# Performance work log

Measured on AMD Instinct MI355X. Metric: run time of the kernel, lower is better.

The kernel has to match this reference:

```python
import jax, jax.numpy as jnp
import numpy as np
import math

B, S, D = 2, 4096, 512
H = 8
DH = D // H  # 64


def setup_inputs() -> dict:
    key = jax.random.key(0)
    k1, k2, k3, k4, k5 = jax.random.split(key, 5)
    scale = 1.0 / math.sqrt(D)
    return {
        "x": jax.random.normal(k1, (B, S, D), dtype=jnp.float32),
        "W_in": jax.random.normal(k2, (D, 3 * D), dtype=jnp.float32) * scale,
        "b_in": jax.random.normal(k3, (3 * D,), dtype=jnp.float32) * 0.01,
        "W_out": jax.random.normal(k4, (D, D), dtype=jnp.float32) * scale,
        "b_out": jax.random.normal(k5, (D,), dtype=jnp.float32) * 0.01,
        "causal_mask": 1,
    }


def reference(x, W_in, b_in, W_out, b_out, causal_mask):
    b, s, d = x.shape
    # fused QKV projection: (b, s, 3d)
    qkv = x @ W_in + b_in
    q, k, v = jnp.split(qkv, 3, axis=-1)
    # (b, s, d) -> (b, h, s, dh)
    def to_heads(t):
        return t.reshape(b, s, H, DH).transpose(0, 2, 1, 3)
    q, k, v = to_heads(q), to_heads(k), to_heads(v)
    # raw scores (b, h, s, s)
    scores = jnp.einsum("bhqd,bhkd->bhqk", q, k)
    if causal_mask:  # static python flag
        # upper-triangular (strictly above diag) -> -inf, applied pre-scaling
        # (matches source; -inf invariant under /sqrt(d_head))
        tri = jnp.triu(jnp.ones((s, s), dtype=bool), k=1)
        scores = jnp.where(tri, -jnp.inf, scores)
    attn = jax.nn.softmax(scores / math.sqrt(DH), axis=-1)
    out = jnp.einsum("bhqk,bhkd->bhqd", attn, v)
    out = out.transpose(0, 2, 1, 3).reshape(b, s, d)
    return out @ W_out + b_out
```

## Files before the change

### kernel.cpp

```cpp
#include <hip/hip_runtime.h>
#include <cstdint>
#include <cmath>

typedef unsigned short BF16;
typedef __attribute__((ext_vector_type(8))) short short8;
typedef __attribute__((ext_vector_type(4))) float f32x4;
typedef __attribute__((ext_vector_type(16))) float f32x16;
typedef __attribute__((ext_vector_type(2))) unsigned int uint2v;
typedef __attribute__((ext_vector_type(4))) unsigned int uint4v;

#define S_LEN 4096
#define DMODEL 512
#define NHEAD 8
#define DHEAD 64
#define BS 2
#define NROWS (BS * NHEAD * S_LEN)

__device__ __forceinline__ BF16 f2bf(float f) {
  union { float f; uint32_t u; } v; v.f = f;
  uint32_t r = (v.u + 0x7FFFu + ((v.u >> 16) & 1u)) >> 16;
  return (BF16)r;
}

__device__ __forceinline__ float bf2f(short u) {
  return __uint_as_float(((unsigned)(unsigned short)u) << 16);
}

__device__ __forceinline__ unsigned cvtpk(float a, float b) {
  unsigned r;
  asm volatile("v_cvt_pk_bf16_f32 %0, %1, %2" : "=v"(r) : "v"(a), "v"(b));
  return r;
}

__device__ __forceinline__ float partner32(float x, int hi) {
  unsigned a = __float_as_uint(x), b = a;
  uint2v r = __builtin_amdgcn_permlane32_swap(a, b, false, false);
  return __uint_as_float(hi ? r[0] : r[1]);
}

__device__ __forceinline__ void pl32(unsigned &a, unsigned &b) {
  uint2v r = __builtin_amdgcn_permlane32_swap(a, b, false, false);
  a = r[0]; b = r[1];
}

__device__ __forceinline__ void gload16(const void* g, void* lds) {
  __builtin_amdgcn_global_load_lds(
      (const __attribute__((address_space(1))) void*)g,
      (__attribute__((address_space(3))) void*)lds, 16, 0, 0);
}

#define MAX3(a, b, c) fmaxf(fmaxf((a), (b)), (c))
#define CS_CONST 0.18033688011112042f

__global__ __launch_bounds__(256) void cvt_x_k(const float* __restrict__ x,
                                               BF16* __restrict__ xb) {
  int i = blockIdx.x * 256 + threadIdx.x;
  float4 v = reinterpret_cast<const float4*>(x)[i];
  ushort4 o;
  o.x = f2bf(v.x); o.y = f2bf(v.y); o.z = f2bf(v.z); o.w = f2bf(v.w);
  reinterpret_cast<ushort4*>(xb)[i] = o;
}

__global__ __launch_bounds__(256) void trw_k(const float* __restrict__ W_in,
                                             const float* __restrict__ W_out,
                                             BF16* __restrict__ wint,
                                             BF16* __restrict__ woutt) {
  __shared__ float t[32][33];
  const bool second = blockIdx.x >= 48;
  const float* W = second ? W_out : W_in;
  BF16* Wt = second ? woutt : wint;
  const int N = second ? DMODEL : 3 * DMODEL;
  const int K = DMODEL;
  int n0 = (second ? ((int)blockIdx.x - 48) : (int)blockIdx.x) * 32;
  int k0 = blockIdx.y * 32;
  int tx = threadIdx.x & 31, ty = threadIdx.x >> 5;
#pragma unroll
  for (int i = 0; i < 4; ++i)
    t[ty + 8 * i][tx] = W[(size_t)(k0 + ty + 8 * i) * N + n0 + tx];
  __syncthreads();
#pragma unroll
  for (int i = 0; i < 4; ++i)
    Wt[(size_t)(n0 + ty + 8 * i) * K + k0 + tx] = f2bf(t[tx][ty + 8 * i]);
}

template <int MODE>
__global__ __launch_bounds__(256)
void gemm_k(const BF16* __restrict__ A, const BF16* __restrict__ Bt,
            const float* __restrict__ bias,
            BF16* __restrict__ Qb, BF16* __restrict__ Kb, BF16* __restrict__ Vc,
            float* __restrict__ Out) {
  __shared__ BF16 As[128 * 64];
  __shared__ BF16 Bs[128 * 64];
  const int tid = threadIdx.x;
  const int l = tid & 63, w = tid >> 6;
  const int wm = w >> 1, wn = w & 1;
  const int bm = blockIdx.x, bn = blockIdx.y;
  f32x4 acc[4][4] = {};

  for (int kt = 0; kt < 512 / 64; ++kt) {
#pragma unroll
    for (int i = 0; i < 4; ++i) {
      int ldsoff = i * 4096 + w * 1024;
      int off = ldsoff + l * 16;
      int row = off >> 7;
      int slot = ((off >> 4) & 7) ^ (row & 7);
      gload16(A + (size_t)(bm * 128 + row) * 512 + kt * 64 + slot * 8,
              (char*)As + ldsoff);
      gload16(Bt + (size_t)(bn * 128 + row) * 512 + kt * 64 + slot * 8,
              (char*)Bs + ldsoff);
    }
    __syncthreads();
    const char* Ab = (const char*)As;
    const char* Bb = (const char*)Bs;
    short8 af[4][2], bfr[4][2];
#pragma unroll
    for (int mf = 0; mf < 4; ++mf)
#pragma unroll
      for (int kk = 0; kk < 2; ++kk) {
        int row = wm * 64 + mf * 16 + (l & 15);
        int slot = ((l >> 4) + 4 * kk) ^ (row & 7);
        af[mf][kk] = *(const short8*)(Ab + row * 128 + slot * 16);
      }
#pragma unroll
    for (int nf = 0; nf < 4; ++nf)
#pragma unroll
      for (int kk = 0; kk < 2; ++kk) {
        int row = wn * 64 + nf * 16 + (l & 15);
        int slot = ((l >> 4) + 4 * kk) ^ (row & 7);
        bfr[nf][kk] = *(const short8*)(Bb + row * 128 + slot * 16);
      }
    __builtin_amdgcn_s_setprio(1);
#pragma unroll
    for (int kk = 0; kk < 2; ++kk)
#pragma unroll
      for (int mf = 0; mf < 4; ++mf)
#pragma unroll
        for (int nf = 0; nf < 4; ++nf)
          acc[mf][nf] = __builtin_amdgcn_mfma_f32_16x16x32_bf16(
              af[mf][kk], bfr[nf][kk], acc[mf][nf], 0, 0, 0);
    __builtin_amdgcn_s_setprio(0);
    __syncthreads();
  }

#pragma unroll
  for (int mf = 0; mf < 4; ++mf)
#pragma unroll
    for (int nf = 0; nf < 4; ++nf)
#pragma unroll
      for (int r = 0; r < 4; ++r) {
        int row = bm * 128 + wm * 64 + mf * 16 + ((l >> 4) << 2) + r;
        int col = bn * 128 + wn * 64 + nf * 16 + (l & 15);
        float v = acc[mf][nf][r] + bias[col];
        if (MODE == 0) {
          int sec = col >> 9, nl = col & 511;
          int h = nl >> 6, dh = nl & 63;
          int b = row >> 12, s = row & 4095;
          BF16* dst = sec == 0 ? Qb : (sec == 1 ? Kb : Vc);
          dst[(((size_t)(b * NHEAD + h)) * S_LEN + s) * DHEAD + dh] = f2bf(v);
        } else {
          Out[(size_t)row * DMODEL + col] = v;
        }
      }
}

__global__ __launch_bounds__(256)
void v_tr_k(const BF16* __restrict__ Vc, BF16* __restrict__ Vt) {
  __shared__ BF16 t[64][66];
  const int bh = blockIdx.y, st = blockIdx.x;
  const int tid = threadIdx.x;
  const int g = tid >> 3, c8 = (tid & 7) * 8;
#pragma unroll
  for (int p = 0; p < 2; ++p) {
    int s = p * 32 + g;
    short8 v = *(const short8*)(Vc + ((size_t)bh * S_LEN + st * 64 + s) * DHEAD + c8);
#pragma unroll
    for (int j = 0; j < 8; ++j) t[s][c8 + j] = (BF16)(unsigned short)v[j];
  }
  __syncthreads();
#pragma unroll
  for (int p = 0; p < 2; ++p) {
    int dh = p * 32 + g;
    short8 o;
#pragma unroll
    for (int j = 0; j < 8; ++j) o[j] = (short)t[c8 + j][dh];
    *(short8*)(Vt + ((size_t)bh * DHEAD + dh) * S_LEN + st * 64 + c8) = o;
  }
}

__global__ __launch_bounds__(256, 4)
void attn_k(const BF16* __restrict__ Qg, const BF16* __restrict__ Kg,
            const BF16* __restrict__ Vg, BF16* __restrict__ Opb,
            float* __restrict__ Ml) {
  __shared__ BF16 Kl[2][64 * 64];
  __shared__ BF16 Vl[2][64 * 64];
  const int tid = threadIdx.x, l = tid & 63, w = tid >> 6;
  const int hi = l >> 5, ln = l & 31;
  const int wgid = blockIdx.x;
  const int xcd = wgid & 7, j = wgid >> 3;
  const int bh = xcd * 2 + (j & 1);
  const int qr = (j >> 1) & 3;
  const int p = j >> 3;
  const BF16* Qh = Qg + (size_t)bh * S_LEN * DHEAD;
  const BF16* Kh = Kg + (size_t)bh * S_LEN * DHEAD;
  const BF16* Vh = Vg + (size_t)bh * DHEAD * S_LEN;
  const float CS = CS_CONST;

  int cur = 0;
  for (int rep = 0; rep < 2; ++rep) {
    const int qt = rep ? (31 - p) : p;
    const int qq = rep ? (3 - qr) : qr;
    const int NTf = 2 * qt + 2;
    const int kbase = (qq * NTf) >> 2;
    const int kend = ((qq + 1) * NTf) >> 2;
    const int NT = kend - kbase;
    const int q0w = qt * 128 + w * 32;
    const int qrow = q0w + ln;
    __syncthreads();

    short8 qb[4];
    {
      const BF16* qp = Qh + (size_t)qrow * DHEAD + hi * 8;
#pragma unroll
      for (int ks = 0; ks < 4; ++ks) qb[ks] = *(const short8*)(qp + ks * 16);
    }
    f32x16 oacc0 = {}, oacc1 = {};
    float m_ = -INFINITY, l_ = 0.f;

    auto stage = [&](int buf, int ktile) {
      const int kv0 = ktile * 64;
#pragma unroll
      for (int i = 0; i < 2; ++i) {
        int base = i * 4096 + w * 1024;
        int off = base + l * 16;
        int row = off >> 7;
        int slot = ((off >> 4) & 7) ^ (row & 7);
        gload16(Kh + (size_t)(kv0 + row) * DHEAD + slot * 8, (char*)Kl[buf] + base);
        gload16(Vh + (size_t)row * S_LEN + kv0 + slot * 8, (char*)Vl[buf] + base);
      }
    };

    if (NT > 0) {
      stage(cur, kbase);
      for (int kt = 0; kt < NT; ++kt) {
        __syncthreads();
        if (kt + 1 < NT) stage(cur ^ 1, kbase + kt + 1);
        const int kv0 = (kbase + kt) * 64;
        if (kv0 <= q0w + 31) {
          const char* Kb_ = (const char*)Kl[cur];
          f32x16 s0 = {}, s1 = {};
          __builtin_amdgcn_s_setprio(1);
#pragma unroll
          for (int ks = 0; ks < 4; ++ks) {
            int slot0 = (2 * ks + hi) ^ (ln & 7);
            short8 kf0 = *(const short8*)(Kb_ + ln * 128 + slot0 * 16);
            int row1 = 32 + ln;
            int slot1 = (2 * ks + hi) ^ (row1 & 7);
            short8 kf1 = *(const short8*)(Kb_ + row1 * 128 + slot1 * 16);
            s0 = __builtin_amdgcn_mfma_f32_32x32x16_bf16(kf0, qb[ks], s0, 0, 0, 0);
            s1 = __builtin_amdgcn_mfma_f32_32x32x16_bf16(kf1, qb[ks], s1, 0, 0, 0);
          }
          __builtin_amdgcn_s_setprio(0);
          if (kv0 + 63 > q0w) {
#pragma unroll
            for (int r = 0; r < 16; ++r) {
              int crow = (r & 3) + 8 * (r >> 2) + 4 * hi;
              if (kv0 + crow > qrow) s0[r] = -INFINITY;
              if (kv0 + 32 + crow > qrow) s1[r] = -INFINITY;
            }
          }
          float a0 = MAX3(s0[0], s0[1], s0[2]);
          float a1 = MAX3(s0[3], s0[4], s0[5]);
          float a2 = MAX3(s0[6], s0[7], s0[8]);
          float a3 = MAX3(s0[9], s0[10], s0[11]);
          float a4 = MAX3(s0[12], s0[13], s0[14]);
          float a5 = MAX3(s0[15], s1[0], s1[1]);
          float a6 = MAX3(s1[2], s1[3], s1[4]);
          float a7 = MAX3(s1[5], s1[6], s1[7]);
          float a8 = MAX3(s1[8], s1[9], s1[10]);
          float a9 = MAX3(s1[11], s1[12], s1[13]);
          float a10 = fmaxf(s1[14], s1[15]);
          float b0 = MAX3(a0, a1, a2);
          float b1 = MAX3(a3, a4, a5);
          float b2 = MAX3(a6, a7, a8);
          float b3 = fmaxf(a9, a10);
          float pmax = fmaxf(fmaxf(b0, b1), fmaxf(b2, b3));
          pmax = fmaxf(pmax, partner32(pmax, hi));
          bool need = (pmax - m_) * CS > 8.0f;
          if (__any(need)) {
            float mn = fmaxf(m_, pmax);
            float alpha = exp2f((m_ - mn) * CS);
            m_ = mn;
            l_ *= alpha;
#pragma unroll
            for (int r = 0; r < 16; ++r) { oacc0[r] *= alpha; oacc1[r] *= alpha; }
          }
          const float mb = m_ * CS;
          float p0[16], p1[16];
          float rs = 0.f;
#pragma unroll
          for (int r = 0; r < 16; ++r) { p0[r] = exp2f(fmaf(s0[r], CS, -mb)); rs += p0[r]; }
#pragma unroll
          for (int r = 0; r < 16; ++r) { p1[r] = exp2f(fmaf(s1[r], CS, -mb)); rs += p1[r]; }
          rs += partner32(rs, hi);
          l_ += rs;
          short8 pf[4];
#pragma unroll
          for (int hf = 0; hf < 2; ++hf) {
            const float* pp = hf ? p1 : p0;
            unsigned w01 = cvtpk(pp[0], pp[1]), w23 = cvtpk(pp[2], pp[3]);
            unsigned w45 = cvtpk(pp[4], pp[5]), w67 = cvtpk(pp[6], pp[7]);
            unsigned w89 = cvtpk(pp[8], pp[9]), wab = cvtpk(pp[10], pp[11]);
            unsigned wcd = cvtpk(pp[12], pp[13]), wef = cvtpk(pp[14], pp[15]);
            pl32(w01, w45);
            pl32(w23, w67);
            pl32(w89, wcd);
            pl32(wab, wef);
            union { uint4v u; short8 s; } c0, c1;
            c0.u = (uint4v){w01, w23, w45, w67};
            c1.u = (uint4v){w89, wab, wcd, wef};
            pf[hf * 2 + 0] = c0.s;
            pf[hf * 2 + 1] = c1.s;
          }
          const char* Vb_ = (const char*)Vl[cur];
          __builtin_amdgcn_s_setprio(1);
#pragma unroll
          for (int ks = 0; ks < 4; ++ks) {
            int slot0 = (2 * ks + hi) ^ (ln & 7);
            short8 vf0 = *(const short8*)(Vb_ + ln * 128 + slot0 * 16);
            int row1 = 32 + ln;
            int slot1 = (2 * ks + hi) ^ (row1 & 7);
            short8 vf1 = *(const short8*)(Vb_ + row1 * 128 + slot1 * 16);
            oacc0 = __builtin_amdgcn_mfma_f32_32x32x16_bf16(vf0, pf[ks], oacc0, 0, 0, 0);
            oacc1 = __builtin_amdgcn_mfma_f32_32x32x16_bf16(vf1, pf[ks], oacc1, 0, 0, 0);
          }
          __builtin_amdgcn_s_setprio(0);
        }
        cur ^= 1;
      }
    }

    BF16* Op = Opb + ((size_t)qq * NROWS + (size_t)bh * S_LEN + qrow) * DHEAD;
#pragma unroll
    for (int blk = 0; blk < 2; ++blk) {
      const f32x16 oa = blk ? oacc1 : oacc0;
#pragma unroll
      for (int g = 0; g < 4; ++g) {
        int dh0 = 8 * g + 4 * hi + 32 * blk;
        unsigned lo = cvtpk(oa[4 * g + 0], oa[4 * g + 1]);
        unsigned h2 = cvtpk(oa[4 * g + 2], oa[4 * g + 3]);
        uint2v st = {lo, h2};
        *(uint2v*)(Op + dh0) = st;
      }
    }
    if (hi == 0) {
      float2 ml = {m_, l_};
      *(float2*)(Ml + ((size_t)qq * NROWS + (size_t)bh * S_LEN + qrow) * 2) = ml;
    }
  }
}

__global__ __launch_bounds__(256)
void merge_k(const BF16* __restrict__ Opb, const float* __restrict__ Ml,
             BF16* __restrict__ Ob) {
  const int wv = blockIdx.x * 4 + (threadIdx.x >> 6);
  const int lane = threadIdx.x & 63;
  const int r_off = lane >> 3, c8 = (lane & 7) * 8;
#pragma unroll
  for (int it = 0; it < 4; ++it) {
    int row = wv * 32 + it * 8 + r_off;
    float2 ml0 = *(const float2*)(Ml + (size_t)row * 2);
    float2 ml1 = *(const float2*)(Ml + ((size_t)NROWS + row) * 2);
    float2 ml2 = *(const float2*)(Ml + ((size_t)2 * NROWS + row) * 2);
    float2 ml3 = *(const float2*)(Ml + ((size_t)3 * NROWS + row) * 2);
    float m = fmaxf(fmaxf(ml0.x, ml1.x), fmaxf(ml2.x, ml3.x));
    float a0 = exp2f((ml0.x - m) * CS_CONST);
    float a1 = exp2f((ml1.x - m) * CS_CONST);
    float a2 = exp2f((ml2.x - m) * CS_CONST);
    float a3 = exp2f((ml3.x - m) * CS_CONST);
    float linv = 1.0f / (ml0.y * a0 + ml1.y * a1 + ml2.y * a2 + ml3.y * a3);
    a0 *= linv; a1 *= linv; a2 *= linv; a3 *= linv;
    short8 v0 = *(const short8*)(Opb + ((size_t)0 * NROWS + row) * DHEAD + c8);
    short8 v1 = *(const short8*)(Opb + ((size_t)1 * NROWS + row) * DHEAD + c8);
    short8 v2 = *(const short8*)(Opb + ((size_t)2 * NROWS + row) * DHEAD + c8);
    short8 v3 = *(const short8*)(Opb + ((size_t)3 * NROWS + row) * DHEAD + c8);
    float o[8];
#pragma unroll
    for (int jj = 0; jj < 8; ++jj)
      o[jj] = bf2f(v0[jj]) * a0 + bf2f(v1[jj]) * a1 +
              bf2f(v2[jj]) * a2 + bf2f(v3[jj]) * a3;
    uint4v pk = {cvtpk(o[0], o[1]), cvtpk(o[2], o[3]),
                 cvtpk(o[4], o[5]), cvtpk(o[6], o[7])};
    int bh = row >> 12, s = row & 4095;
    *(uint4v*)(Ob + ((size_t)((bh >> 3) * S_LEN + s)) * DMODEL +
               (bh & 7) * DHEAD + c8) = pk;
  }
}

extern "C" void kernel_launch(void* const* d_in, const int* in_sizes, int n_in,
                              void* d_out, int out_size, void* d_ws, size_t ws_size,
                              hipStream_t stream) {
  const float* x = (const float*)d_in[0];
  const float* W_in = (const float*)d_in[1];
  const float* b_in = (const float*)d_in[2];
  const float* W_out = (const float*)d_in[3];
  const float* b_out = (const float*)d_in[4];
  float* out = (float*)d_out;

  char* ws = (char*)d_ws;
  const size_t SZ_X = (size_t)BS * S_LEN * DMODEL * 2;
  const size_t SZ_OP = (size_t)NROWS * DHEAD * 2;
  BF16* xb    = (BF16*)(ws);
  BF16* Vt    = xb;
  BF16* wint  = (BF16*)(ws + SZ_X);
  BF16* woutt = (BF16*)(ws + SZ_X + 3 * DMODEL * DMODEL * 2);
  BF16* Qb    = (BF16*)(ws + SZ_X + 4 * DMODEL * DMODEL * 2);
  BF16* Kb    = (BF16*)((char*)Qb + SZ_X);
  BF16* Vc    = (BF16*)((char*)Kb + SZ_X);
  BF16* Ob    = (BF16*)((char*)Vc + SZ_X);
  BF16* Opb   = (BF16*)((char*)Ob + SZ_X);
  float* Ml   = (float*)((char*)Opb + 4 * SZ_OP);

  cvt_x_k<<<dim3((BS * S_LEN * DMODEL) / 4 / 256), 256, 0, stream>>>(x, xb);
  trw_k<<<dim3(64, DMODEL / 32), 256, 0, stream>>>(W_in, W_out, wint, woutt);
  gemm_k<0><<<dim3(BS * S_LEN / 128, 3 * DMODEL / 128), 256, 0, stream>>>(
      xb, wint, b_in, Qb, Kb, Vc, nullptr);
  v_tr_k<<<dim3(S_LEN / 64, BS * NHEAD), 256, 0, stream>>>(Vc, Vt);
  attn_k<<<dim3(1024), 256, 0, stream>>>(Qb, Kb, Vt, Opb, Ml);
  merge_k<<<dim3(512), 256, 0, stream>>>(Opb, Ml, Ob);
  gemm_k<1><<<dim3(BS * S_LEN / 128, DMODEL / 128), 256, 0, stream>>>(
      Ob, woutt, b_out, nullptr, nullptr, nullptr, out);
}
```

Baseline: 193.7 us.

## Fuse V transpose into QKV GEMM epilogue and merge prep kernels

The QKV GEMM now writes V directly in transposed (head, dh, seq) layout. It stages each V tile through the A/B shared-memory buffers and stores 16-byte vectors, which removes the separate v_tr_k kernel and its round trip through global memory. The x conversion and weight transpose kernels are merged into one launch, saving a kernel launch. The workspace layout is reshuffled so Ob aliases xb. The risk is extra LDS traffic and a barrier in the V-block epilogue.

```diff
diff --git a/kernel.cpp b/kernel.cpp
--- a/kernel.cpp
+++ b/kernel.cpp
@@ -52,27 +52,29 @@
 #define MAX3(a, b, c) fmaxf(fmaxf((a), (b)), (c))
 #define CS_CONST 0.18033688011112042f
 
-__global__ __launch_bounds__(256) void cvt_x_k(const float* __restrict__ x,
-                                               BF16* __restrict__ xb) {
-  int i = blockIdx.x * 256 + threadIdx.x;
-  float4 v = reinterpret_cast<const float4*>(x)[i];
-  ushort4 o;
-  o.x = f2bf(v.x); o.y = f2bf(v.y); o.z = f2bf(v.z); o.w = f2bf(v.w);
-  reinterpret_cast<ushort4*>(xb)[i] = o;
-}
-
-__global__ __launch_bounds__(256) void trw_k(const float* __restrict__ W_in,
-                                             const float* __restrict__ W_out,
-                                             BF16* __restrict__ wint,
-                                             BF16* __restrict__ woutt) {
+__global__ __launch_bounds__(256)
+void prep_k(const float* __restrict__ x, const float* __restrict__ W_in,
+            const float* __restrict__ W_out, BF16* __restrict__ xb,
+            BF16* __restrict__ wint, BF16* __restrict__ woutt) {
   __shared__ float t[32][33];
-  const bool second = blockIdx.x >= 48;
+  const int bx = blockIdx.x;
+  if (bx < 4096) {
+    int i = bx * 256 + threadIdx.x;
+    float4 v = reinterpret_cast<const float4*>(x)[i];
+    ushort4 o;
+    o.x = f2bf(v.x); o.y = f2bf(v.y); o.z = f2bf(v.z); o.w = f2bf(v.w);
+    reinterpret_cast<ushort4*>(xb)[i] = o;
+    return;
+  }
+  const int tb = bx - 4096;
+  const int bxx = tb & 63, byy = tb >> 6;
+  const bool second = bxx >= 48;
   const float* W = second ? W_out : W_in;
   BF16* Wt = second ? woutt : wint;
   const int N = second ? DMODEL : 3 * DMODEL;
   const int K = DMODEL;
-  int n0 = (second ? ((int)blockIdx.x - 48) : (int)blockIdx.x) * 32;
-  int k0 = blockIdx.y * 32;
+  int n0 = (second ? (bxx - 48) : bxx) * 32;
+  int k0 = byy * 32;
   int tx = threadIdx.x & 31, ty = threadIdx.x >> 5;
 #pragma unroll
   for (int i = 0; i < 4; ++i)
@@ -87,7 +89,7 @@
 __global__ __launch_bounds__(256)
 void gemm_k(const BF16* __restrict__ A, const BF16* __restrict__ Bt,
             const float* __restrict__ bias,
-            BF16* __restrict__ Qb, BF16* __restrict__ Kb, BF16* __restrict__ Vc,
+            BF16* __restrict__ Qb, BF16* __restrict__ Kb, BF16* __restrict__ Vt,
             float* __restrict__ Out) {
   __shared__ BF16 As[128 * 64];
   __shared__ BF16 Bs[128 * 64];
@@ -142,6 +144,39 @@
     __syncthreads();
   }
 
+  if (MODE == 0 && bn >= 8) {
+#pragma unroll
+    for (int mf = 0; mf < 4; ++mf)
+#pragma unroll
+      for (int nf = 0; nf < 4; ++nf)
+#pragma unroll
+        for (int r = 0; r < 4; ++r) {
+          int rloc = wm * 64 + mf * 16 + ((l >> 4) << 2) + r;
+          int col = bn * 128 + wn * 64 + nf * 16 + (l & 15);
+          float v = acc[mf][nf][r] + bias[col];
+          int nl = col & 511;
+          int hh = (nl >> 6) & 1;
+          int dh = nl & 63;
+          BF16* T = hh ? Bs : As;
+          T[dh * 128 + rloc] = f2bf(v);
+        }
+    __syncthreads();
+    const int dh_grp = tid >> 4;
+    const int soff = (tid & 15) * 8;
+    const int b = bm >> 5, s0 = (bm & 31) * 128;
+#pragma unroll
+    for (int it = 0; it < 8; ++it) {
+      int dhh = it * 16 + dh_grp;
+      int head = dhh >> 6, dh = dhh & 63;
+      const BF16* T = head ? Bs : As;
+      short8 vv = *(const short8*)(T + dh * 128 + soff);
+      int hglob = (bn - 8) * 2 + head;
+      *(short8*)(Vt + (((size_t)(b * NHEAD + hglob)) * DHEAD + dh) * S_LEN +
+                 s0 + soff) = vv;
+    }
+    return;
+  }
+
 #pragma unroll
   for (int mf = 0; mf < 4; ++mf)
 #pragma unroll
@@ -155,36 +190,12 @@
           int sec = col >> 9, nl = col & 511;
           int h = nl >> 6, dh = nl & 63;
           int b = row >> 12, s = row & 4095;
-          BF16* dst = sec == 0 ? Qb : (sec == 1 ? Kb : Vc);
+          BF16* dst = sec == 0 ? Qb : Kb;
           dst[(((size_t)(b * NHEAD + h)) * S_LEN + s) * DHEAD + dh] = f2bf(v);
         } else {
           Out[(size_t)row * DMODEL + col] = v;
         }
       }
-}
-
-__global__ __launch_bounds__(256)
-void v_tr_k(const BF16* __restrict__ Vc, BF16* __restrict__ Vt) {
-  __shared__ BF16 t[64][66];
-  const int bh = blockIdx.y, st = blockIdx.x;
-  const int tid = threadIdx.x;
-  const int g = tid >> 3, c8 = (tid & 7) * 8;
-#pragma unroll
-  for (int p = 0; p < 2; ++p) {
-    int s = p * 32 + g;
-    short8 v = *(const short8*)(Vc + ((size_t)bh * S_LEN + st * 64 + s) * DHEAD + c8);
-#pragma unroll
-    for (int j = 0; j < 8; ++j) t[s][c8 + j] = (BF16)(unsigned short)v[j];
-  }
-  __syncthreads();
-#pragma unroll
-  for (int p = 0; p < 2; ++p) {
-    int dh = p * 32 + g;
-    short8 o;
-#pragma unroll
-    for (int j = 0; j < 8; ++j) o[j] = (short)t[c8 + j][dh];
-    *(short8*)(Vt + ((size_t)bh * DHEAD + dh) * S_LEN + st * 64 + c8) = o;
-  }
 }
 
 __global__ __launch_bounds__(256, 4)
@@ -410,21 +421,18 @@
   const size_t SZ_X = (size_t)BS * S_LEN * DMODEL * 2;
   const size_t SZ_OP = (size_t)NROWS * DHEAD * 2;
   BF16* xb    = (BF16*)(ws);
-  BF16* Vt    = xb;
+  BF16* Ob    = xb;
   BF16* wint  = (BF16*)(ws + SZ_X);
   BF16* woutt = (BF16*)(ws + SZ_X + 3 * DMODEL * DMODEL * 2);
   BF16* Qb    = (BF16*)(ws + SZ_X + 4 * DMODEL * DMODEL * 2);
   BF16* Kb    = (BF16*)((char*)Qb + SZ_X);
-  BF16* Vc    = (BF16*)((char*)Kb + SZ_X);
-  BF16* Ob    = (BF16*)((char*)Vc + SZ_X);
-  BF16* Opb   = (BF16*)((char*)Ob + SZ_X);
+  BF16* Vt    = (BF16*)((char*)Kb + SZ_X);
+  BF16* Opb   = (BF16*)((char*)Vt + SZ_X);
   float* Ml   = (float*)((char*)Opb + 4 * SZ_OP);
 
-  cvt_x_k<<<dim3((BS * S_LEN * DMODEL) / 4 / 256), 256, 0, stream>>>(x, xb);
-  trw_k<<<dim3(64, DMODEL / 32), 256, 0, stream>>>(W_in, W_out, wint, woutt);
+  prep_k<<<dim3(4096 + 1024), 256, 0, stream>>>(x, W_in, W_out, xb, wint, woutt);
   gemm_k<0><<<dim3(BS * S_LEN / 128, 3 * DMODEL / 128), 256, 0, stream>>>(
-      xb, wint, b_in, Qb, Kb, Vc, nullptr);
-  v_tr_k<<<dim3(S_LEN / 64, BS * NHEAD), 256, 0, stream>>>(Vc, Vt);
+      xb, wint, b_in, Qb, Kb, Vt, nullptr);
   attn_k<<<dim3(1024), 256, 0, stream>>>(Qb, Kb, Vt, Opb, Ml);
   merge_k<<<dim3(512), 256, 0, stream>>>(Opb, Ml, Ob);
   gemm_k<1><<<dim3(BS * S_LEN / 128, DMODEL / 128), 256, 0, stream>>>(
```

Result: faster. 187.4 us (-3.2%).
